# Kernel tuning notes

Hardware: AMD Instinct MI355X
Metric: run time of the kernel (lower is better)

## Reference

```python
import jax, jax.numpy as jnp
import numpy as np

MIN = 1e-30
BLOCK = 64


def setup_inputs() -> dict:
    key = jax.random.key(0)
    ks = jax.random.split(key, 16)
    B, L, D, H, M, E, P, R = 4, 512, 768, 12, 48, 32, 512, 97
    inp = {
        "context": jax.random.normal(ks[0], (B, L, D), jnp.float32),
        "attention": jax.random.uniform(ks[1], (B, H, L, L), jnp.float32),
        "mention_map": jax.random.uniform(ks[2], (B, M, L), jnp.float32),
        "entity_map": jax.random.uniform(ks[3], (B, E, M), jnp.float32),
        "hts": jax.random.randint(ks[4], (B, P, 2), 0, E).astype(jnp.int64),
        "hW": jax.random.normal(ks[5], (D, D), jnp.float32) * 0.02,
        "hb": jnp.zeros((D,), jnp.float32),
        "tW": jax.random.normal(ks[6], (D, D), jnp.float32) * 0.02,
        "tb": jnp.zeros((D,), jnp.float32),
        "hcW": jax.random.normal(ks[7], (D, D), jnp.float32) * 0.02,
        "hcb": jnp.zeros((D,), jnp.float32),
        "tcW": jax.random.normal(ks[8], (D, D), jnp.float32) * 0.02,
        "tcb": jnp.zeros((D,), jnp.float32),
        "clasW": jax.random.normal(ks[9], (R, D * BLOCK), jnp.float32) * 0.02,
        "clasb": jnp.zeros((R,), jnp.float32),
    }
    return inp


def _group_bilinear(h, t, W, b):
    # h, t: [B, P, D]; grouped bilinear a la ATLOP: block-outer-product then linear
    B, P, D = h.shape
    nb = D // BLOCK
    h_ = h.reshape(B, P, nb, BLOCK)
    t_ = t.reshape(B, P, nb, BLOCK)
    feat = jnp.einsum("bpni,bpnj->bpnij", h_, t_).reshape(B, P, D * BLOCK)
    return feat @ W.T + b


def _forward(context, attention, mention_map, entity_map, hts,
             hW, hb, tW, tb, hcW, hcb, tcW, tcb, clasW, clasb):
    B = context.shape[0]
    bidx = jnp.arange(B)[:, None]
    h_idx = hts[..., 0]  # [B, P]
    t_idx = hts[..., 1]
    ht_mask = (hts.sum(-1) != 0)[..., None].astype(context.dtype)  # [B, P, 1]

    # ---- get_ht ----
    mention = mention_map @ context                       # [B, M, D]
    att_sum = attention.sum(axis=1)                       # [B, L, L]
    mention_att = mention_map @ att_sum @ jnp.swapaxes(mention_map, 1, 2)  # [B, M, M]
    entity_att = entity_map @ mention_att                 # [B, E, M]

    h_mask = entity_map[bidx, h_idx] * ht_mask            # [B, P, M]
    t_mask = entity_map[bidx, t_idx] * ht_mask
    h_att = entity_att[bidx, h_idx] * t_mask
    t_att = entity_att[bidx, t_idx] * h_mask
    h_att = h_att / (h_att.sum(-1, keepdims=True) + MIN)
    t_att = t_att / (t_att.sum(-1, keepdims=True) + MIN)
    h = (t_att @ mention) * ht_mask                       # [B, P, D]
    t = (h_att @ mention) * ht_mask

    # ---- context_pooling (entity_map projected to token space) ----
    em_tok = entity_map @ mention_map                     # [B, E, L]
    em_tok = em_tok / (em_tok.sum(-1, keepdims=True) + MIN)
    ent_att = jnp.einsum("bel,bhlm->bhem", em_tok, attention)  # [B, H, E, L]
    hA = ent_att[bidx, :, h_idx]                          # [B, P, H, L]
    tA = ent_att[bidx, :, t_idx]
    ctx_att = (hA * tA).sum(axis=2)                       # [B, P, L]
    ctx_att = ctx_att / (ctx_att.sum(-1, keepdims=True) + MIN)
    context_info = (ctx_att @ context) * ht_mask          # [B, P, D]

    h_info = context_info @ hcW.T + hcb
    t_info = context_info @ tcW.T + tcb
    h = jnp.tanh(h @ hW.T + hb + h_info)
    t = jnp.tanh(t @ tW.T + tb + t_info)
    return _group_bilinear(h, t, clasW, clasb)            # [B, P, R]


def reference(context, attention, mention_map, entity_map, hts,
              hW, hb, tW, tb, hcW, hcb, tcW, tcb, clasW, clasb):
    return _forward(context, attention, mention_map, entity_map, hts,
                    hW, hb, tW, tb, hcW, hcb, tcW, tcb, clasW, clasb)
```

## Files before the change

kernel.cpp:

```cpp
#include <hip/hip_runtime.h>
#include <math.h>

#define Bc 4
#define Lc 512
#define Dc 768
#define Hc 12
#define Mc 48
#define Ec 32
#define Pc 512
#define Rc 97
#define MINV 1e-30f

typedef _Float16 f16;
typedef __attribute__((ext_vector_type(8))) _Float16 f16x8;
typedef __attribute__((ext_vector_type(4))) _Float16 f16x4;
typedef __attribute__((ext_vector_type(16))) float f32x16;

__global__ __launch_bounds__(256) void k_prep(const float* __restrict__ hW, const float* __restrict__ tW,
                                              const float* __restrict__ hcW, const float* __restrict__ tcW,
                                              f16* __restrict__ hWb, f16* __restrict__ tWb,
                                              f16* __restrict__ hcWb, f16* __restrict__ tcWb,
                                              const float* __restrict__ clasW, f16* __restrict__ Wp,
                                              const float* __restrict__ ctx, f16* __restrict__ ctxT,
                                              const float* __restrict__ mm, f16* __restrict__ mmH) {
    __shared__ f16 Ts[64][72];
    int bid = blockIdx.x;
    int tid = threadIdx.x;
    if (bid < 2048) {
        const int DD = Dc * Dc;
        int i = bid * 256 + tid;
        int stride = 2048 * 256;
        for (; i < 4 * DD; i += stride) {
            int sel = i / DD, j = i % DD;
            const float* s = (sel == 0) ? hW : (sel == 1) ? tW : (sel == 2) ? hcW : tcW;
            f16* d = (sel == 0) ? hWb : (sel == 1) ? tWb : (sel == 2) ? hcWb : tcWb;
            d[j] = (f16)s[j];
        }
    } else if (bid < 5120) {
        int gid = (bid - 2048) * 256 + tid;
        int lane = gid & 63; int f = gid >> 6;
        int rt = f & 3; int s = (f >> 2) & 3; int c = f >> 4;
        int n_l = lane & 31, kg = lane >> 5;
        int r = rt * 32 + n_l;
        f16x8 v;
        if (r < Rc) {
            const float* src = clasW + (size_t)r * (Dc * 64) + c * 64 + s * 16 + kg * 8;
#pragma unroll
            for (int j = 0; j < 8; ++j) v[j] = (f16)src[j];
        } else {
#pragma unroll
            for (int j = 0; j < 8; ++j) v[j] = (f16)0.f;
        }
        ((f16x8*)Wp)[gid] = v;
    } else if (bid < 5504) {
        int id = bid - 5120;
        int dt = id % 12; int lt = (id / 12) % 8; int b = id / 96;
        int l0 = lt * 64, d0 = dt * 64;
        int r = tid >> 2, cg = tid & 3;
        const float* src = ctx + ((size_t)b * Lc + l0 + r) * Dc + d0 + cg * 16;
#pragma unroll
        for (int u = 0; u < 4; ++u) {
            float4 v = ((const float4*)src)[u];
            Ts[cg * 16 + u * 4 + 0][r] = (f16)v.x;
            Ts[cg * 16 + u * 4 + 1][r] = (f16)v.y;
            Ts[cg * 16 + u * 4 + 2][r] = (f16)v.z;
            Ts[cg * 16 + u * 4 + 3][r] = (f16)v.w;
        }
        __syncthreads();
        int dr = tid >> 2, seg = tid & 3;
        f16* dst = ctxT + ((size_t)b * Dc + d0 + dr) * Lc + l0 + seg * 16;
        f16x8 o0, o1;
#pragma unroll
        for (int j = 0; j < 8; ++j) { o0[j] = Ts[dr][seg * 16 + j]; o1[j] = Ts[dr][seg * 16 + 8 + j]; }
        *(f16x8*)dst = o0;
        *(f16x8*)(dst + 8) = o1;
    } else {
        int gid = (bid - 5504) * 256 + tid;
        const float4* src = (const float4*)(mm + (size_t)gid * 8);
        float4 v0 = src[0], v1 = src[1];
        f16x8 o;
        o[0] = (f16)v0.x; o[1] = (f16)v0.y; o[2] = (f16)v0.z; o[3] = (f16)v0.w;
        o[4] = (f16)v1.x; o[5] = (f16)v1.y; o[6] = (f16)v1.z; o[7] = (f16)v1.w;
        ((f16x8*)mmH)[gid] = o;
    }
}

__global__ __launch_bounds__(256) void k_mention_mfma(const f16* __restrict__ mmH,
                                                      const f16* __restrict__ ctxT,
                                                      float* __restrict__ mention) {
    __shared__ __align__(16) f16 As[2][64 * 64];
    __shared__ __align__(16) f16 Bs[2][64 * 64];
    int id = blockIdx.x;
    int dt = id % 12; int b = id / 12;
    int d0 = dt * 64;
    int tid = threadIdx.x;
    int w = tid >> 6, lane = tid & 63;
    int w_m = w & 1, w_n = w >> 1;
    int m_l = lane & 31, kg = lane >> 5;
    int r0 = tid >> 3, cc0 = tid & 7;
    int r1 = r0 + 32;
    int mr0 = (r0 < Mc) ? r0 : r0 - Mc;
    int mr1 = (r1 < Mc) ? r1 : r1 - Mc;
    f16x8 ar0, ar1, br0, br1;
    auto loadt = [&](int it) {
        int k0 = it * 64;
        ar0 = *(const f16x8*)(mmH + ((size_t)b * Mc + mr0) * Lc + k0 + cc0 * 8);
        ar1 = *(const f16x8*)(mmH + ((size_t)b * Mc + mr1) * Lc + k0 + cc0 * 8);
        br0 = *(const f16x8*)(ctxT + ((size_t)b * Dc + d0 + r0) * Lc + k0 + cc0 * 8);
        br1 = *(const f16x8*)(ctxT + ((size_t)b * Dc + d0 + r1) * Lc + k0 + cc0 * 8);
    };
    auto writet = [&](int p) {
        ((f16x8*)As[p])[r0 * 8 + (cc0 ^ (r0 & 7))] = ar0;
        ((f16x8*)As[p])[r1 * 8 + (cc0 ^ (r1 & 7))] = ar1;
        ((f16x8*)Bs[p])[r0 * 8 + (cc0 ^ (r0 & 7))] = br0;
        ((f16x8*)Bs[p])[r1 * 8 + (cc0 ^ (r1 & 7))] = br1;
    };
    loadt(0); writet(0); loadt(1);
    f32x16 acc;
#pragma unroll
    for (int i = 0; i < 16; ++i) acc[i] = 0.f;
    int ar = w_m * 32 + m_l;
    int br = w_n * 32 + m_l;
    for (int it = 0; it < 8; ++it) {
        int p = it & 1;
        __syncthreads();
        if (it < 7) writet(p ^ 1);
        if (it < 6) loadt(it + 2);
#pragma unroll
        for (int s = 0; s < 4; ++s) {
            int ck = s * 2 + kg;
            f16x8 a = ((const f16x8*)As[p])[ar * 8 + (ck ^ (ar & 7))];
            f16x8 bv = ((const f16x8*)Bs[p])[br * 8 + (ck ^ (br & 7))];
            acc = __builtin_amdgcn_mfma_f32_32x32x16_f16(a, bv, acc, 0, 0, 0);
        }
    }
#pragma unroll
    for (int reg = 0; reg < 16; ++reg) {
        int row = (reg & 3) + 8 * (reg >> 2) + 4 * kg;
        int m = w_m * 32 + row;
        if (m < Mc) mention[((size_t)b * Mc + m) * Dc + d0 + w_n * 32 + m_l] = acc[reg];
    }
}

__global__ __launch_bounds__(256) void k_attpass(const f16* __restrict__ mmH,
                                                 const f16* __restrict__ emtH,
                                                 const float* __restrict__ att,
                                                 float* __restrict__ tmpML,
                                                 float* __restrict__ eat) {
    __shared__ __align__(16) f16 Ss[96 * 64];
    __shared__ __align__(16) f16 attS[64 * 64];
    int id = blockIdx.x;
    int mt = id & 7; int bh = id >> 3;
    int b = bh / Hc, h = bh % Hc;
    int m0 = mt * 64;
    int tid = threadIdx.x;
    int w = tid >> 6, lane = tid & 63;
    int n_l = lane & 31, kg = lane >> 5;

    const float* ab = att + (size_t)bh * Lc * Lc + m0;
    int mRow = tid & 63, lg = tid >> 6;
    float pre[16];
#pragma unroll
    for (int q = 0; q < 16; ++q) pre[q] = ab[(size_t)(lg * 16 + q) * Lc + mRow];

    f32x16 acc[2];
#pragma unroll
    for (int nt = 0; nt < 2; ++nt)
#pragma unroll
        for (int i = 0; i < 16; ++i) acc[nt][i] = 0.f;

    for (int kc = 0; kc < 8; ++kc) {
        __syncthreads();
#pragma unroll
        for (int half = 0; half < 2; ++half) {
            int cc = lg * 2 + half;
            f16x8 v;
#pragma unroll
            for (int jj = 0; jj < 8; ++jj) v[jj] = (f16)pre[half * 8 + jj];
            ((f16x8*)attS)[mRow * 8 + (cc ^ (mRow & 7))] = v;
        }
#pragma unroll
        for (int k = 0; k < 3; ++k) {
            int idx = tid + k * 256;
            int row = idx >> 3, cc = idx & 7;
            f16x8 v;
            if (row < Mc) {
                v = *(const f16x8*)(mmH + ((size_t)b * Mc + row) * Lc + kc * 64 + cc * 8);
            } else if (row < 80) {
                v = *(const f16x8*)(emtH + ((size_t)b * Ec + row - Mc) * Lc + kc * 64 + cc * 8);
            } else {
#pragma unroll
                for (int j = 0; j < 8; ++j) v[j] = (f16)0.f;
            }
            ((f16x8*)Ss)[row * 8 + (cc ^ (row & 7))] = v;
        }
        if (kc < 7) {
#pragma unroll
            for (int q = 0; q < 16; ++q)
                pre[q] = ab[(size_t)((kc + 1) * 64 + lg * 16 + q) * Lc + mRow];
        }
        __syncthreads();
        if (w < 3) {
            int arow = w * 32 + n_l;
#pragma unroll
            for (int kk = 0; kk < 4; ++kk) {
                int cc = kk * 2 + kg;
                f16x8 a = ((const f16x8*)Ss)[arow * 8 + (cc ^ (arow & 7))];
#pragma unroll
                for (int nt = 0; nt < 2; ++nt) {
                    int bcol = nt * 32 + n_l;
                    f16x8 bb = ((const f16x8*)attS)[bcol * 8 + (cc ^ (bcol & 7))];
                    acc[nt] = __builtin_amdgcn_mfma_f32_32x32x16_f16(a, bb, acc[nt], 0, 0, 0);
                }
            }
        }
    }
    if (w < 3) {
#pragma unroll
        for (int nt = 0; nt < 2; ++nt)
#pragma unroll
            for (int reg = 0; reg < 16; ++reg) {
                int row = (reg & 3) + 8 * (reg >> 2) + 4 * kg;
                int rr = w * 32 + row;
                int col = m0 + nt * 32 + n_l;
                if (rr < Mc) {
                    atomicAdd(&tmpML[((size_t)b * Mc + rr) * Lc + col], acc[nt][reg]);
                } else if (rr < 80) {
                    eat[(((size_t)b * Hc + h) * Ec + (rr - Mc)) * Lc + col] = acc[nt][reg];
                }
            }
    }
}

__global__ __launch_bounds__(256) void k_ma(const float* __restrict__ tmp,
                                            const float* __restrict__ mm,
                                            float* __restrict__ maS) {
    int wv = threadIdx.x >> 6, lane = threadIdx.x & 63;
    int gid = blockIdx.x * 4 + wv;
    int m2 = gid % 48;
    int m  = (gid / 48) % 48;
    int b  = gid / (48 * 48);
    const float4* t = (const float4*)(tmp + ((size_t)b * Mc + m)  * Lc);
    const float4* r = (const float4*)(mm  + ((size_t)b * Mc + m2) * Lc);
    float4 a0 = t[lane],      b0 = r[lane];
    float4 a1 = t[lane + 64], b1 = r[lane + 64];
    float acc = a0.x * b0.x + a0.y * b0.y + a0.z * b0.z + a0.w * b0.w
              + a1.x * b1.x + a1.y * b1.y + a1.z * b1.z + a1.w * b1.w;
#pragma unroll
    for (int off = 1; off < 64; off <<= 1) acc += __shfl_xor(acc, off);
    if (lane == 0) maS[gid] = acc;
}

__global__ __launch_bounds__(256) void k_ea(const float* __restrict__ maS,
                                            const float* __restrict__ em,
                                            float* __restrict__ ea) {
    __shared__ float S[48 * 48];
    int b  = blockIdx.x >> 3;
    int eg = blockIdx.x & 7;
    int tid = threadIdx.x;
    for (int i = tid; i < 48 * 48; i += 256) S[i] = maS[(size_t)b * 48 * 48 + i];
    __syncthreads();
    int wv = tid >> 6, lane = tid & 63;
    int e = eg * 4 + wv;
    if (lane < 48) {
        const float* emr = em + ((size_t)b * Ec + e) * Mc;
        float acc = 0.f;
#pragma unroll
        for (int m = 0; m < 48; ++m) acc += emr[m] * S[m * 48 + lane];
        ea[((size_t)b * Ec + e) * Mc + lane] = acc;
    }
}

__global__ __launch_bounds__(256) void k_pair(const int* __restrict__ hts,
                                              const float* __restrict__ em,
                                              const float* __restrict__ ea,
                                              const float* __restrict__ eat,
                                              f16* __restrict__ hatN, f16* __restrict__ tatN,
                                              f16* __restrict__ caH) {
    int wv = threadIdx.x >> 6, lane = threadIdx.x & 63;
    int bp = blockIdx.x * 4 + wv;
    int b = bp >> 9;
    int hi = hts[bp * 2], ti = hts[bp * 2 + 1];
    float mask = (hi + ti != 0) ? 1.f : 0.f;
    float hat = 0.f, tat = 0.f;
    if (lane < Mc) {
        float hm = em[((size_t)(b * Ec + hi)) * Mc + lane];
        float tm = em[((size_t)(b * Ec + ti)) * Mc + lane];
        float eh = ea[((size_t)(b * Ec + hi)) * Mc + lane];
        float et = ea[((size_t)(b * Ec + ti)) * Mc + lane];
        hat = eh * tm * mask;
        tat = et * hm * mask;
    }
    float sh = hat, st = tat;
#pragma unroll
    for (int off = 1; off < 64; off <<= 1) { sh += __shfl_xor(sh, off); st += __shfl_xor(st, off); }
    float hnorm = 1.f / (sh + MINV);
    float tnorm = 1.f / (st + MINV);
    hatN[(size_t)bp * 64 + lane] = (f16)(hat * hnorm);
    tatN[(size_t)bp * 64 + lane] = (f16)(tat * tnorm);

    const float* base = eat + (size_t)b * Hc * Ec * Lc;
    float prod[8];
    float tot = 0.f;
#pragma unroll
    for (int j8 = 0; j8 < 8; ++j8) {
        int j = j8 * 64 + lane;
        float a = 0.f;
#pragma unroll
        for (int h = 0; h < Hc; ++h)
            a += base[((size_t)h * Ec + hi) * Lc + j] * base[((size_t)h * Ec + ti) * Lc + j];
        prod[j8] = a;
        tot += a;
    }
#pragma unroll
    for (int off = 1; off < 64; off <<= 1) tot += __shfl_xor(tot, off);
    float inv = 1.f / (tot + MINV);
#pragma unroll
    for (int j8 = 0; j8 < 8; ++j8)
        caH[(size_t)bp * Lc + j8 * 64 + lane] = (f16)(prod[j8] * inv);
}

__global__ __launch_bounds__(256) void k_ht_mfma(const f16* __restrict__ tatN, const f16* __restrict__ hatN,
                                                 const float* __restrict__ mention,
                                                 f16* __restrict__ hB, f16* __restrict__ tB) {
    __shared__ __align__(16) f16 At[64 * 64];
    __shared__ __align__(16) f16 Ah[64 * 64];
    __shared__ __align__(16) f16 Bs[64 * 64];
    int m0 = blockIdx.x * 64;
    int b = m0 >> 9;
    int d0 = blockIdx.y * 64;
    int tid = threadIdx.x;
    int w = tid >> 6, lane = tid & 63;
    int w_m = w & 1, w_n = w >> 1;
    int m_l = lane & 31, kg = lane >> 5;

    for (int i = tid; i < 512; i += 256) {
        int p = i >> 3, c = i & 7;
        ((f16x8*)At)[p * 8 + (c ^ (p & 7))] = *(const f16x8*)(tatN + (size_t)(m0 + p) * 64 + c * 8);
        ((f16x8*)Ah)[p * 8 + (c ^ (p & 7))] = *(const f16x8*)(hatN + (size_t)(m0 + p) * 64 + c * 8);
    }
    for (int i = tid; i < 512; i += 256) {
        f16x8 z;
#pragma unroll
        for (int j = 0; j < 8; ++j) z[j] = (f16)0.f;
        ((f16x8*)Bs)[i] = z;
    }
    __syncthreads();
    if (tid < 192) {
        int m = tid >> 2, q = tid & 3;
        const float4* src = (const float4*)(mention + ((size_t)b * Mc + m) * Dc + d0 + q * 16);
#pragma unroll
        for (int u = 0; u < 4; ++u) {
            float4 v = src[u];
            int dl = q * 16 + u * 4;
#pragma unroll
            for (int x = 0; x < 4; ++x) {
                float vv = (x == 0) ? v.x : (x == 1) ? v.y : (x == 2) ? v.z : v.w;
                int d = dl + x;
                Bs[(d * 8 + ((m >> 3) ^ (d & 7))) * 8 + (m & 7)] = (f16)vv;
            }
        }
    }
    __syncthreads();

    f32x16 acch, acct;
#pragma unroll
    for (int i = 0; i < 16; ++i) { acch[i] = 0.f; acct[i] = 0.f; }
    int ar = w_m * 32 + m_l;
    int br = w_n * 32 + m_l;
#pragma unroll
    for (int s = 0; s < 4; ++s) {
        int ck = s * 2 + kg;
        f16x8 at_ = ((const f16x8*)At)[ar * 8 + (ck ^ (ar & 7))];
        f16x8 ah_ = ((const f16x8*)Ah)[ar * 8 + (ck ^ (ar & 7))];
        f16x8 bv = ((const f16x8*)Bs)[br * 8 + (ck ^ (br & 7))];
        acch = __builtin_amdgcn_mfma_f32_32x32x16_f16(at_, bv, acch, 0, 0, 0);
        acct = __builtin_amdgcn_mfma_f32_32x32x16_f16(ah_, bv, acct, 0, 0, 0);
    }
#pragma unroll
    for (int reg = 0; reg < 16; ++reg) {
        int row = (reg & 3) + 8 * (reg >> 2) + 4 * kg;
        int p = m0 + w_m * 32 + row;
        int d = d0 + w_n * 32 + m_l;
        hB[(size_t)p * Dc + d] = (f16)acch[reg];
        tB[(size_t)p * Dc + d] = (f16)acct[reg];
    }
}

__global__ __launch_bounds__(256) void k_emtok(const float* __restrict__ em,
                                               const float* __restrict__ mm,
                                               f16* __restrict__ emtH) {
    int be = blockIdx.x; int b = be / Ec;
    __shared__ float row[Mc];
    __shared__ float red[256];
    __shared__ float inv;
    int tid = threadIdx.x;
    if (tid < Mc) row[tid] = em[(size_t)be * Mc + tid];
    __syncthreads();
    float v0 = 0.f, v1 = 0.f;
    {
        const float* mb0 = mm + (size_t)b * Mc * Lc + tid;
        const float* mb1 = mm + (size_t)b * Mc * Lc + tid + 256;
        for (int m = 0; m < Mc; ++m) {
            v0 += row[m] * mb0[(size_t)m * Lc];
            v1 += row[m] * mb1[(size_t)m * Lc];
        }
    }
    red[tid] = v0 + v1;
    __syncthreads();
    for (int s = 128; s > 0; s >>= 1) { if (tid < s) red[tid] += red[tid + s]; __syncthreads(); }
    if (tid == 0) inv = 1.f / (red[0] + MINV);
    __syncthreads();
    emtH[(size_t)be * Lc + tid] = (f16)(v0 * inv);
    emtH[(size_t)be * Lc + tid + 256] = (f16)(v1 * inv);
}

__global__ __launch_bounds__(256) void k_ctxinfo_mfma(const int* __restrict__ hts,
                                                      const f16* __restrict__ caH,
                                                      const f16* __restrict__ ctxT,
                                                      f16* __restrict__ ci) {
    __shared__ __align__(16) f16 As[2][64 * 64];
    __shared__ __align__(16) f16 Bs[2][64 * 64];
    __shared__ float maskS[64];
    int id = blockIdx.x;
    int dt = id % 12; int pt = (id / 12) % 8; int b = id / 96;
    int p0 = pt * 64, d0 = dt * 64;
    int tid = threadIdx.x;
    int w = tid >> 6, lane = tid & 63;
    int w_m = w & 1, w_n = w >> 1;
    int m_l = lane & 31, kg = lane >> 5;
    int r0 = tid >> 3, cc0 = tid & 7;
    int r1 = r0 + 32;
    if (tid < 64) {
        int bp = b * Pc + p0 + tid;
        maskS[tid] = (hts[bp * 2] + hts[bp * 2 + 1] != 0) ? 1.f : 0.f;
    }
    f16x8 ar0, ar1, br0, br1;
    auto loadt = [&](int it) {
        int k0 = it * 64;
        ar0 = *(const f16x8*)(caH + (size_t)(b * Pc + p0 + r0) * Lc + k0 + cc0 * 8);
        ar1 = *(const f16x8*)(caH + (size_t)(b * Pc + p0 + r1) * Lc + k0 + cc0 * 8);
        br0 = *(const f16x8*)(ctxT + (size_t)(b * Dc + d0 + r0) * Lc + k0 + cc0 * 8);
        br1 = *(const f16x8*)(ctxT + (size_t)(b * Dc + d0 + r1) * Lc + k0 + cc0 * 8);
    };
    auto writet = [&](int p) {
        ((f16x8*)As[p])[r0 * 8 + (cc0 ^ (r0 & 7))] = ar0;
        ((f16x8*)As[p])[r1 * 8 + (cc0 ^ (r1 & 7))] = ar1;
        ((f16x8*)Bs[p])[r0 * 8 + (cc0 ^ (r0 & 7))] = br0;
        ((f16x8*)Bs[p])[r1 * 8 + (cc0 ^ (r1 & 7))] = br1;
    };
    loadt(0); writet(0); loadt(1);
    f32x16 acc;
#pragma unroll
    for (int i = 0; i < 16; ++i) acc[i] = 0.f;
    int ar = w_m * 32 + m_l;
    int br = w_n * 32 + m_l;
    for (int it = 0; it < 8; ++it) {
        int p = it & 1;
        __syncthreads();
        if (it < 7) writet(p ^ 1);
        if (it < 6) loadt(it + 2);
#pragma unroll
        for (int s = 0; s < 4; ++s) {
            int ck = s * 2 + kg;
            f16x8 a = ((const f16x8*)As[p])[ar * 8 + (ck ^ (ar & 7))];
            f16x8 bv = ((const f16x8*)Bs[p])[br * 8 + (ck ^ (br & 7))];
            acc = __builtin_amdgcn_mfma_f32_32x32x16_f16(a, bv, acc, 0, 0, 0);
        }
    }
#pragma unroll
    for (int reg = 0; reg < 16; ++reg) {
        int row = (reg & 3) + 8 * (reg >> 2) + 4 * kg;
        int p = p0 + w_m * 32 + row;
        int d = d0 + w_n * 32 + m_l;
        ci[(size_t)(b * Pc + p) * Dc + d] = (f16)(acc[reg] * maskS[w_m * 32 + row]);
    }
}

__global__ __launch_bounds__(256) void k_proj_mfma(const f16* __restrict__ Xh, const f16* __restrict__ Wh,
                                                   const float* __restrict__ bh,
                                                   const f16* __restrict__ Xt, const f16* __restrict__ Wt,
                                                   const float* __restrict__ bt,
                                                   const f16* __restrict__ Xc, const f16* __restrict__ Whc,
                                                   const float* __restrict__ bhc,
                                                   const f16* __restrict__ Wtc, const float* __restrict__ btc,
                                                   f16* __restrict__ outh, f16* __restrict__ outt) {
    __shared__ __align__(16) f16 Xs[2][64 * 64];
    __shared__ __align__(16) f16 Ws[2][64 * 64];
    int z = blockIdx.z;
    const f16* X1 = z ? Xt : Xh;
    const f16* W1 = z ? Wt : Wh;
    const float* b1 = z ? bt : bh;
    const f16* W2 = z ? Wtc : Whc;
    const float* b2 = z ? btc : bhc;
    f16* outp = z ? outt : outh;
    int m0 = blockIdx.x * 64, n0 = blockIdx.y * 64;
    int tid = threadIdx.x;
    int w = tid >> 6, lane = tid & 63;
    int w_m = w & 1, w_n = w >> 1;
    int m_l = lane & 31, kg = lane >> 5;
    const f16* Xarr[2] = {X1, Xc};
    const f16* Warr[2] = {W1, W2};
    int r0 = tid >> 3, cc0 = tid & 7;
    int r1 = r0 + 32;
    f16x8 xr0, xr1, wr0, wr1;
    auto loadt = [&](int it) {
        int src = it / 12; int k0 = (it % 12) * 64;
        const f16* X = Xarr[src]; const f16* W = Warr[src];
        xr0 = *(const f16x8*)(X + (size_t)(m0 + r0) * Dc + k0 + cc0 * 8);
        xr1 = *(const f16x8*)(X + (size_t)(m0 + r1) * Dc + k0 + cc0 * 8);
        wr0 = *(const f16x8*)(W + (size_t)(n0 + r0) * Dc + k0 + cc0 * 8);
        wr1 = *(const f16x8*)(W + (size_t)(n0 + r1) * Dc + k0 + cc0 * 8);
    };
    auto writet = [&](int p) {
        ((f16x8*)Xs[p])[r0 * 8 + (cc0 ^ (r0 & 7))] = xr0;
        ((f16x8*)Xs[p])[r1 * 8 + (cc0 ^ (r1 & 7))] = xr1;
        ((f16x8*)Ws[p])[r0 * 8 + (cc0 ^ (r0 & 7))] = wr0;
        ((f16x8*)Ws[p])[r1 * 8 + (cc0 ^ (r1 & 7))] = wr1;
    };
    loadt(0); writet(0); loadt(1);
    f32x16 acc;
#pragma unroll
    for (int i = 0; i < 16; ++i) acc[i] = 0.f;
    int ar = w_m * 32 + m_l;
    int br = w_n * 32 + m_l;
    for (int it = 0; it < 24; ++it) {
        int p = it & 1;
        __syncthreads();
        if (it < 23) writet(p ^ 1);
        if (it < 22) loadt(it + 2);
#pragma unroll
        for (int s = 0; s < 4; ++s) {
            int ck = s * 2 + kg;
            f16x8 a = ((const f16x8*)Xs[p])[ar * 8 + (ck ^ (ar & 7))];
            f16x8 b = ((const f16x8*)Ws[p])[br * 8 + (ck ^ (br & 7))];
            acc = __builtin_amdgcn_mfma_f32_32x32x16_f16(a, b, acc, 0, 0, 0);
        }
    }
#pragma unroll
    for (int reg = 0; reg < 16; ++reg) {
        int row = (reg & 3) + 8 * (reg >> 2) + 4 * kg;
        int m = m0 + w_m * 32 + row;
        int n = n0 + w_n * 32 + m_l;
        float v = tanhf(acc[reg] + b1[n] + b2[n]);
        outp[(size_t)m * Dc + n] = (f16)v;
    }
}

__global__ __launch_bounds__(256, 3) void k_bilin6(const f16* __restrict__ hF, const f16* __restrict__ tF,
                                                   const f16* __restrict__ Wp, f16* __restrict__ partial) {
    __shared__ __align__(16) f16 tS[128 * 64];
    __shared__ f16 hS[128 * 17];
    int id = blockIdx.x;
    int tile = id / 48;
    int slice = id % 48;
    int bp0 = tile * 128;
    int tid = threadIdx.x;
    int w = tid >> 6, lane = tid & 63;
    int w_m = w & 1, w_r = w >> 1;
    int m_l = lane & 31, kg = lane >> 5;
    int c0 = slice * 16;
    int n = c0 >> 6;

    for (int idx = tid; idx < 128 * 16; idx += 256) {
        int bp = idx >> 4, i = idx & 15;
        hS[bp * 17 + i] = hF[(size_t)(bp0 + bp) * Dc + c0 + i];
    }
    for (int idx = tid; idx < 128 * 8; idx += 256) {
        int bp = idx >> 3, cc = idx & 7;
        f16x8 tv = *(const f16x8*)(tF + (size_t)(bp0 + bp) * Dc + n * 64 + cc * 8);
        ((f16x8*)tS)[bp * 8 + (cc ^ (bp & 7))] = tv;
    }
    __syncthreads();

    f32x16 acc[2][2];
#pragma unroll
    for (int mt = 0; mt < 2; ++mt)
#pragma unroll
        for (int rt = 0; rt < 2; ++rt)
#pragma unroll
            for (int i = 0; i < 16; ++i) acc[mt][rt][i] = 0.f;

    int rowA = w_m * 64 + m_l;
    int rowB = rowA + 32;
    const f16x8* WpB = (const f16x8*)Wp;

    for (int ii = 0; ii < 16; ++ii) {
        int cc = c0 + ii;
        const f16x8* wpb = WpB + (size_t)cc * 16 * 64 + lane;
        f16x8 Bf[8];
#pragma unroll
        for (int s = 0; s < 4; ++s) {
            Bf[s * 2 + 0] = wpb[(s * 4 + 2 * w_r + 0) * 64];
            Bf[s * 2 + 1] = wpb[(s * 4 + 2 * w_r + 1) * 64];
        }
        f16 hv0 = hS[rowA * 17 + ii];
        f16 hv1 = hS[rowB * 17 + ii];
#pragma unroll
        for (int s = 0; s < 4; ++s) {
            int ck = s * 2 + kg;
            f16x8 tv0 = ((const f16x8*)tS)[rowA * 8 + (ck ^ (rowA & 7))];
            f16x8 tv1 = ((const f16x8*)tS)[rowB * 8 + (ck ^ (rowB & 7))];
            f16x8 a0 = tv0 * hv0;
            f16x8 a1 = tv1 * hv1;
            acc[0][0] = __builtin_amdgcn_mfma_f32_32x32x16_f16(a0, Bf[s * 2 + 0], acc[0][0], 0, 0, 0);
            acc[1][0] = __builtin_amdgcn_mfma_f32_32x32x16_f16(a1, Bf[s * 2 + 0], acc[1][0], 0, 0, 0);
            acc[0][1] = __builtin_amdgcn_mfma_f32_32x32x16_f16(a0, Bf[s * 2 + 1], acc[0][1], 0, 0, 0);
            acc[1][1] = __builtin_amdgcn_mfma_f32_32x32x16_f16(a1, Bf[s * 2 + 1], acc[1][1], 0, 0, 0);
        }
    }

    f16* pbase = partial + (size_t)slice * (2048 * 128);
#pragma unroll
    for (int rt = 0; rt < 2; ++rt) {
        int r = (w_r * 2 + rt) * 32 + m_l;
#pragma unroll
        for (int mt = 0; mt < 2; ++mt)
#pragma unroll
            for (int reg = 0; reg < 16; ++reg) {
                int row = (reg & 3) + 8 * (reg >> 2) + 4 * kg;
                int bp = bp0 + w_m * 64 + mt * 32 + row;
                pbase[(size_t)bp * 128 + r] = (f16)acc[mt][rt][reg];
            }
    }
}

__global__ __launch_bounds__(256) void k_reduce(const f16* __restrict__ partial,
                                                const float* __restrict__ cb,
                                                float* __restrict__ out) {
    int idx = blockIdx.x * 256 + threadIdx.x;
    int bp = idx >> 5, c = idx & 31;
    const f16x4* p = (const f16x4*)partial + idx;
    float a0 = 0.f, a1 = 0.f, a2 = 0.f, a3 = 0.f;
#pragma unroll
    for (int s = 0; s < 48; ++s) {
        f16x4 v = p[(size_t)s * (2048 * 32)];
        a0 += (float)v[0]; a1 += (float)v[1]; a2 += (float)v[2]; a3 += (float)v[3];
    }
    int rb = c * 4;
    float* ob = out + (size_t)bp * Rc;
    if (rb + 0 < Rc) ob[rb + 0] = a0 + cb[rb + 0];
    if (rb + 1 < Rc) ob[rb + 1] = a1 + cb[rb + 1];
    if (rb + 2 < Rc) ob[rb + 2] = a2 + cb[rb + 2];
    if (rb + 3 < Rc) ob[rb + 3] = a3 + cb[rb + 3];
}

extern "C" void kernel_launch(void* const* d_in, const int* in_sizes, int n_in,
                              void* d_out, int out_size, void* d_ws, size_t ws_size,
                              hipStream_t stream) {
    const float* context   = (const float*)d_in[0];
    const float* attention = (const float*)d_in[1];
    const float* mm        = (const float*)d_in[2];
    const float* em        = (const float*)d_in[3];
    const int*   hts       = (const int*)d_in[4];
    const float* hW        = (const float*)d_in[5];
    const float* hb        = (const float*)d_in[6];
    const float* tW        = (const float*)d_in[7];
    const float* tb        = (const float*)d_in[8];
    const float* hcW       = (const float*)d_in[9];
    const float* hcb       = (const float*)d_in[10];
    const float* tcW       = (const float*)d_in[11];
    const float* tcb       = (const float*)d_in[12];
    const float* clasW     = (const float*)d_in[13];
    const float* clasb     = (const float*)d_in[14];
    float* out = (float*)d_out;

    char* wsb = (char*)d_ws;
    auto alloc = [&](size_t bytes) { char* p = wsb; wsb += (bytes + 255) & ~(size_t)255; return p; };
    float* mention     = (float*)alloc((size_t)Bc * Mc * Dc * 4);
    float* tmpML       = (float*)alloc((size_t)Bc * Mc * Lc * 4);
    float* entity_att  = (float*)alloc((size_t)Bc * Ec * Mc * 4);
    float* ent_att     = (float*)alloc((size_t)Bc * Hc * Ec * Lc * 4);
    float* maS         = (float*)alloc((size_t)Bc * Mc * Mc * 4);
    f16* em_tok  = (f16*)alloc((size_t)Bc * Ec * Lc * 2);
    f16* ctx_att = (f16*)alloc((size_t)Bc * Pc * Lc * 2);
    f16* mmH     = (f16*)alloc((size_t)Bc * Mc * Lc * 2);
    f16* hatN    = (f16*)alloc((size_t)Bc * Pc * 64 * 2);
    f16* tatN    = (f16*)alloc((size_t)Bc * Pc * 64 * 2);
    f16* h_buf   = (f16*)alloc((size_t)Bc * Pc * Dc * 2);
    f16* t_buf   = (f16*)alloc((size_t)Bc * Pc * Dc * 2);
    f16* ctxinfo = (f16*)alloc((size_t)Bc * Pc * Dc * 2);
    f16* h_fin   = (f16*)alloc((size_t)Bc * Pc * Dc * 2);
    f16* t_fin   = (f16*)alloc((size_t)Bc * Pc * Dc * 2);
    f16* hWb     = (f16*)alloc((size_t)Dc * Dc * 2);
    f16* tWb     = (f16*)alloc((size_t)Dc * Dc * 2);
    f16* hcWb    = (f16*)alloc((size_t)Dc * Dc * 2);
    f16* tcWb    = (f16*)alloc((size_t)Dc * Dc * 2);
    f16* ctxT    = (f16*)alloc((size_t)Bc * Dc * Lc * 2);
    f16* Wp      = (f16*)alloc((size_t)768 * 16 * 64 * 8 * 2);
    f16* partial = (f16*)alloc((size_t)48 * 2048 * 128 * 2);

    hipMemsetAsync(tmpML, 0, (size_t)Bc * Mc * Lc * 4, stream);
    k_prep<<<dim3(5552), dim3(256), 0, stream>>>(hW, tW, hcW, tcW, hWb, tWb, hcWb, tcWb,
                                                 clasW, Wp, context, ctxT, mm, mmH);
    k_emtok<<<dim3(Bc * Ec), dim3(256), 0, stream>>>(em, mm, em_tok);
    k_attpass<<<dim3(Bc * Hc * 8), dim3(256), 0, stream>>>(mmH, em_tok, attention, tmpML, ent_att);
    k_mention_mfma<<<dim3(Bc * 12), dim3(256), 0, stream>>>(mmH, ctxT, mention);
    k_ma<<<dim3(Bc * Mc * Mc / 4), dim3(256), 0, stream>>>(tmpML, mm, maS);
    k_ea<<<dim3(Bc * 8), dim3(256), 0, stream>>>(maS, em, entity_att);
    k_pair<<<dim3(Bc * Pc / 4), dim3(256), 0, stream>>>(hts, em, entity_att, ent_att, hatN, tatN, ctx_att);
    k_ht_mfma<<<dim3(32, 12), dim3(256), 0, stream>>>(tatN, hatN, mention, h_buf, t_buf);
    k_ctxinfo_mfma<<<dim3(384), dim3(256), 0, stream>>>(hts, ctx_att, ctxT, ctxinfo);
    k_proj_mfma<<<dim3(32, 12, 2), dim3(256), 0, stream>>>(h_buf, hWb, hb, t_buf, tWb, tb,
                                                           ctxinfo, hcWb, hcb, tcWb, tcb, h_fin, t_fin);
    k_bilin6<<<dim3(768), dim3(256), 0, stream>>>(h_fin, t_fin, Wp, partial);
    k_reduce<<<dim3(256), dim3(256), 0, stream>>>(partial, clasb, out);
}
```

Measured before the change: 265.8 us.

## Merge independent kernels into shared launches and retile bilinear kernel

```diff
diff --git a/kernel.cpp b/kernel.cpp
--- a/kernel.cpp
+++ b/kernel.cpp
@@ -10,6 +10,7 @@
 #define Pc 512
 #define Rc 97
 #define MINV 1e-30f
+#define NSLICE 24
 
 typedef _Float16 f16;
 typedef __attribute__((ext_vector_type(8))) _Float16 f16x8;
@@ -22,8 +23,12 @@
                                               f16* __restrict__ hcWb, f16* __restrict__ tcWb,
                                               const float* __restrict__ clasW, f16* __restrict__ Wp,
                                               const float* __restrict__ ctx, f16* __restrict__ ctxT,
-                                              const float* __restrict__ mm, f16* __restrict__ mmH) {
+                                              const float* __restrict__ mm, f16* __restrict__ mmH,
+                                              const float* __restrict__ em, f16* __restrict__ emtH) {
     __shared__ f16 Ts[64][72];
+    __shared__ float rowS[Mc];
+    __shared__ float red[256];
+    __shared__ float inv;
     int bid = blockIdx.x;
     int tid = threadIdx.x;
     if (bid < 2048) {
@@ -74,7 +79,7 @@
         for (int j = 0; j < 8; ++j) { o0[j] = Ts[dr][seg * 16 + j]; o1[j] = Ts[dr][seg * 16 + 8 + j]; }
         *(f16x8*)dst = o0;
         *(f16x8*)(dst + 8) = o1;
-    } else {
+    } else if (bid < 5552) {
         int gid = (bid - 5504) * 256 + tid;
         const float4* src = (const float4*)(mm + (size_t)gid * 8);
         float4 v0 = src[0], v1 = src[1];
@@ -82,153 +87,172 @@
         o[0] = (f16)v0.x; o[1] = (f16)v0.y; o[2] = (f16)v0.z; o[3] = (f16)v0.w;
         o[4] = (f16)v1.x; o[5] = (f16)v1.y; o[6] = (f16)v1.z; o[7] = (f16)v1.w;
         ((f16x8*)mmH)[gid] = o;
-    }
-}
-
-__global__ __launch_bounds__(256) void k_mention_mfma(const f16* __restrict__ mmH,
-                                                      const f16* __restrict__ ctxT,
-                                                      float* __restrict__ mention) {
-    __shared__ __align__(16) f16 As[2][64 * 64];
-    __shared__ __align__(16) f16 Bs[2][64 * 64];
-    int id = blockIdx.x;
-    int dt = id % 12; int b = id / 12;
-    int d0 = dt * 64;
+    } else {
+        int be = bid - 5552; int b = be / Ec;
+        if (tid < Mc) rowS[tid] = em[(size_t)be * Mc + tid];
+        __syncthreads();
+        float v0 = 0.f, v1 = 0.f;
+        {
+            const float* mb0 = mm + (size_t)b * Mc * Lc + tid;
+            const float* mb1 = mm + (size_t)b * Mc * Lc + tid + 256;
+            for (int m = 0; m < Mc; ++m) {
+                v0 += rowS[m] * mb0[(size_t)m * Lc];
+                v1 += rowS[m] * mb1[(size_t)m * Lc];
+            }
+        }
+        red[tid] = v0 + v1;
+        __syncthreads();
+        for (int s = 128; s > 0; s >>= 1) { if (tid < s) red[tid] += red[tid + s]; __syncthreads(); }
+        if (tid == 0) inv = 1.f / (red[0] + MINV);
+        __syncthreads();
+        emtH[(size_t)be * Lc + tid] = (f16)(v0 * inv);
+        emtH[(size_t)be * Lc + tid + 256] = (f16)(v1 * inv);
+    }
+}
+
+__global__ __launch_bounds__(256) void k_att_mention(const f16* __restrict__ mmH,
+                                                     const f16* __restrict__ emtH,
+                                                     const float* __restrict__ att,
+                                                     float* __restrict__ tmpML,
+                                                     float* __restrict__ eat,
+                                                     const f16* __restrict__ ctxT,
+                                                     float* __restrict__ mention) {
+    __shared__ __align__(16) char smem[32768];
+    int bid = blockIdx.x;
     int tid = threadIdx.x;
     int w = tid >> 6, lane = tid & 63;
-    int w_m = w & 1, w_n = w >> 1;
-    int m_l = lane & 31, kg = lane >> 5;
-    int r0 = tid >> 3, cc0 = tid & 7;
-    int r1 = r0 + 32;
-    int mr0 = (r0 < Mc) ? r0 : r0 - Mc;
-    int mr1 = (r1 < Mc) ? r1 : r1 - Mc;
-    f16x8 ar0, ar1, br0, br1;
-    auto loadt = [&](int it) {
-        int k0 = it * 64;
-        ar0 = *(const f16x8*)(mmH + ((size_t)b * Mc + mr0) * Lc + k0 + cc0 * 8);
-        ar1 = *(const f16x8*)(mmH + ((size_t)b * Mc + mr1) * Lc + k0 + cc0 * 8);
-        br0 = *(const f16x8*)(ctxT + ((size_t)b * Dc + d0 + r0) * Lc + k0 + cc0 * 8);
-        br1 = *(const f16x8*)(ctxT + ((size_t)b * Dc + d0 + r1) * Lc + k0 + cc0 * 8);
-    };
-    auto writet = [&](int p) {
-        ((f16x8*)As[p])[r0 * 8 + (cc0 ^ (r0 & 7))] = ar0;
-        ((f16x8*)As[p])[r1 * 8 + (cc0 ^ (r1 & 7))] = ar1;
-        ((f16x8*)Bs[p])[r0 * 8 + (cc0 ^ (r0 & 7))] = br0;
-        ((f16x8*)Bs[p])[r1 * 8 + (cc0 ^ (r1 & 7))] = br1;
-    };
-    loadt(0); writet(0); loadt(1);
-    f32x16 acc;
-#pragma unroll
-    for (int i = 0; i < 16; ++i) acc[i] = 0.f;
-    int ar = w_m * 32 + m_l;
-    int br = w_n * 32 + m_l;
-    for (int it = 0; it < 8; ++it) {
-        int p = it & 1;
-        __syncthreads();
-        if (it < 7) writet(p ^ 1);
-        if (it < 6) loadt(it + 2);
-#pragma unroll
-        for (int s = 0; s < 4; ++s) {
-            int ck = s * 2 + kg;
-            f16x8 a = ((const f16x8*)As[p])[ar * 8 + (ck ^ (ar & 7))];
-            f16x8 bv = ((const f16x8*)Bs[p])[br * 8 + (ck ^ (br & 7))];
-            acc = __builtin_amdgcn_mfma_f32_32x32x16_f16(a, bv, acc, 0, 0, 0);
-        }
-    }
-#pragma unroll
-    for (int reg = 0; reg < 16; ++reg) {
-        int row = (reg & 3) + 8 * (reg >> 2) + 4 * kg;
-        int m = w_m * 32 + row;
-        if (m < Mc) mention[((size_t)b * Mc + m) * Dc + d0 + w_n * 32 + m_l] = acc[reg];
-    }
-}
-
-__global__ __launch_bounds__(256) void k_attpass(const f16* __restrict__ mmH,
-                                                 const f16* __restrict__ emtH,
-                                                 const float* __restrict__ att,
-                                                 float* __restrict__ tmpML,
-                                                 float* __restrict__ eat) {
-    __shared__ __align__(16) f16 Ss[96 * 64];
-    __shared__ __align__(16) f16 attS[64 * 64];
-    int id = blockIdx.x;
-    int mt = id & 7; int bh = id >> 3;
-    int b = bh / Hc, h = bh % Hc;
-    int m0 = mt * 64;
-    int tid = threadIdx.x;
-    int w = tid >> 6, lane = tid & 63;
-    int n_l = lane & 31, kg = lane >> 5;
-
-    const float* ab = att + (size_t)bh * Lc * Lc + m0;
-    int mRow = tid & 63, lg = tid >> 6;
-    float pre[16];
-#pragma unroll
-    for (int q = 0; q < 16; ++q) pre[q] = ab[(size_t)(lg * 16 + q) * Lc + mRow];
-
-    f32x16 acc[2];
-#pragma unroll
-    for (int nt = 0; nt < 2; ++nt)
-#pragma unroll
-        for (int i = 0; i < 16; ++i) acc[nt][i] = 0.f;
-
-    for (int kc = 0; kc < 8; ++kc) {
-        __syncthreads();
-#pragma unroll
-        for (int half = 0; half < 2; ++half) {
-            int cc = lg * 2 + half;
-            f16x8 v;
-#pragma unroll
-            for (int jj = 0; jj < 8; ++jj) v[jj] = (f16)pre[half * 8 + jj];
-            ((f16x8*)attS)[mRow * 8 + (cc ^ (mRow & 7))] = v;
-        }
-#pragma unroll
-        for (int k = 0; k < 3; ++k) {
-            int idx = tid + k * 256;
-            int row = idx >> 3, cc = idx & 7;
-            f16x8 v;
-            if (row < Mc) {
-                v = *(const f16x8*)(mmH + ((size_t)b * Mc + row) * Lc + kc * 64 + cc * 8);
-            } else if (row < 80) {
-                v = *(const f16x8*)(emtH + ((size_t)b * Ec + row - Mc) * Lc + kc * 64 + cc * 8);
-            } else {
-#pragma unroll
-                for (int j = 0; j < 8; ++j) v[j] = (f16)0.f;
-            }
-            ((f16x8*)Ss)[row * 8 + (cc ^ (row & 7))] = v;
-        }
-        if (kc < 7) {
-#pragma unroll
-            for (int q = 0; q < 16; ++q)
-                pre[q] = ab[(size_t)((kc + 1) * 64 + lg * 16 + q) * Lc + mRow];
-        }
-        __syncthreads();
+    if (bid < 384) {
+        f16* Ss   = (f16*)smem;
+        f16* attS = (f16*)(smem + 12288);
+        int mt = bid & 7; int bh = bid >> 3;
+        int b = bh / Hc, h = bh % Hc;
+        int m0 = mt * 64;
+        int n_l = lane & 31, kg = lane >> 5;
+
+        const float* ab = att + (size_t)bh * Lc * Lc + m0;
+        int mRow = tid & 63, lg = tid >> 6;
+        float pre[16];
+#pragma unroll
+        for (int q = 0; q < 16; ++q) pre[q] = ab[(size_t)(lg * 16 + q) * Lc + mRow];
+
+        f32x16 acc[2];
+#pragma unroll
+        for (int nt = 0; nt < 2; ++nt)
+#pragma unroll
+            for (int i = 0; i < 16; ++i) acc[nt][i] = 0.f;
+
+        for (int kc = 0; kc < 8; ++kc) {
+            __syncthreads();
+#pragma unroll
+            for (int half = 0; half < 2; ++half) {
+                int cc = lg * 2 + half;
+                f16x8 v;
+#pragma unroll
+                for (int jj = 0; jj < 8; ++jj) v[jj] = (f16)pre[half * 8 + jj];
+                ((f16x8*)attS)[mRow * 8 + (cc ^ (mRow & 7))] = v;
+            }
+#pragma unroll
+            for (int k = 0; k < 3; ++k) {
+                int idx = tid + k * 256;
+                int row = idx >> 3, cc = idx & 7;
+                f16x8 v;
+                if (row < Mc) {
+                    v = *(const f16x8*)(mmH + ((size_t)b * Mc + row) * Lc + kc * 64 + cc * 8);
+                } else if (row < 80) {
+                    v = *(const f16x8*)(emtH + ((size_t)b * Ec + row - Mc) * Lc + kc * 64 + cc * 8);
+                } else {
+#pragma unroll
+                    for (int j = 0; j < 8; ++j) v[j] = (f16)0.f;
+                }
+                ((f16x8*)Ss)[row * 8 + (cc ^ (row & 7))] = v;
+            }
+            if (kc < 7) {
+#pragma unroll
+                for (int q = 0; q < 16; ++q)
+                    pre[q] = ab[(size_t)((kc + 1) * 64 + lg * 16 + q) * Lc + mRow];
+            }
+            __syncthreads();
+            if (w < 3) {
+                int arow = w * 32 + n_l;
+#pragma unroll
+                for (int kk = 0; kk < 4; ++kk) {
+                    int cc = kk * 2 + kg;
+                    f16x8 a = ((const f16x8*)Ss)[arow * 8 + (cc ^ (arow & 7))];
+#pragma unroll
+                    for (int nt = 0; nt < 2; ++nt) {
+                        int bcol = nt * 32 + n_l;
+                        f16x8 bb = ((const f16x8*)attS)[bcol * 8 + (cc ^ (bcol & 7))];
+                        acc[nt] = __builtin_amdgcn_mfma_f32_32x32x16_f16(a, bb, acc[nt], 0, 0, 0);
+                    }
+                }
+            }
+        }
         if (w < 3) {
-            int arow = w * 32 + n_l;
-#pragma unroll
-            for (int kk = 0; kk < 4; ++kk) {
-                int cc = kk * 2 + kg;
-                f16x8 a = ((const f16x8*)Ss)[arow * 8 + (cc ^ (arow & 7))];
-#pragma unroll
-                for (int nt = 0; nt < 2; ++nt) {
-                    int bcol = nt * 32 + n_l;
-                    f16x8 bb = ((const f16x8*)attS)[bcol * 8 + (cc ^ (bcol & 7))];
-                    acc[nt] = __builtin_amdgcn_mfma_f32_32x32x16_f16(a, bb, acc[nt], 0, 0, 0);
+#pragma unroll
+            for (int nt = 0; nt < 2; ++nt)
+#pragma unroll
+                for (int reg = 0; reg < 16; ++reg) {
+                    int row = (reg & 3) + 8 * (reg >> 2) + 4 * kg;
+                    int rr = w * 32 + row;
+                    int col = m0 + nt * 32 + n_l;
+                    if (rr < Mc) {
+                        atomicAdd(&tmpML[((size_t)b * Mc + rr) * Lc + col], acc[nt][reg]);
+                    } else if (rr < 80) {
+                        eat[(((size_t)b * Hc + h) * Ec + (rr - Mc)) * Lc + col] = acc[nt][reg];
+                    }
                 }
-            }
-        }
-    }
-    if (w < 3) {
-#pragma unroll
-        for (int nt = 0; nt < 2; ++nt)
-#pragma unroll
-            for (int reg = 0; reg < 16; ++reg) {
-                int row = (reg & 3) + 8 * (reg >> 2) + 4 * kg;
-                int rr = w * 32 + row;
-                int col = m0 + nt * 32 + n_l;
-                if (rr < Mc) {
-                    atomicAdd(&tmpML[((size_t)b * Mc + rr) * Lc + col], acc[nt][reg]);
-                } else if (rr < 80) {
-                    eat[(((size_t)b * Hc + h) * Ec + (rr - Mc)) * Lc + col] = acc[nt][reg];
-                }
-            }
+        }
+    } else {
+        f16* As = (f16*)smem;
+        f16* Bs = (f16*)(smem + 16384);
+        int id = bid - 384;
+        int dt = id % 12; int b = id / 12;
+        int d0 = dt * 64;
+        int w_m = w & 1, w_n = w >> 1;
+        int m_l = lane & 31, kg = lane >> 5;
+        int r0 = tid >> 3, cc0 = tid & 7;
+        int r1 = r0 + 32;
+        int mr0 = (r0 < Mc) ? r0 : r0 - Mc;
+        int mr1 = (r1 < Mc) ? r1 : r1 - Mc;
+        f16x8 ar0, ar1, br0, br1;
+        auto loadt = [&](int it) {
+            int k0 = it * 64;
+            ar0 = *(const f16x8*)(mmH + ((size_t)b * Mc + mr0) * Lc + k0 + cc0 * 8);
+            ar1 = *(const f16x8*)(mmH + ((size_t)b * Mc + mr1) * Lc + k0 + cc0 * 8);
+            br0 = *(const f16x8*)(ctxT + ((size_t)b * Dc + d0 + r0) * Lc + k0 + cc0 * 8);
+            br1 = *(const f16x8*)(ctxT + ((size_t)b * Dc + d0 + r1) * Lc + k0 + cc0 * 8);
+        };
+        auto writet = [&](int p) {
+            ((f16x8*)(As + p * 4096))[r0 * 8 + (cc0 ^ (r0 & 7))] = ar0;
+            ((f16x8*)(As + p * 4096))[r1 * 8 + (cc0 ^ (r1 & 7))] = ar1;
+            ((f16x8*)(Bs + p * 4096))[r0 * 8 + (cc0 ^ (r0 & 7))] = br0;
+            ((f16x8*)(Bs + p * 4096))[r1 * 8 + (cc0 ^ (r1 & 7))] = br1;
+        };
+        loadt(0); writet(0); loadt(1);
+        f32x16 acc;
+#pragma unroll
+        for (int i = 0; i < 16; ++i) acc[i] = 0.f;
+        int ar = w_m * 32 + m_l;
+        int br = w_n * 32 + m_l;
+        for (int it = 0; it < 8; ++it) {
+            int p = it & 1;
+            __syncthreads();
+            if (it < 7) writet(p ^ 1);
+            if (it < 6) loadt(it + 2);
+#pragma unroll
+            for (int s = 0; s < 4; ++s) {
+                int ck = s * 2 + kg;
+                f16x8 a = ((const f16x8*)(As + p * 4096))[ar * 8 + (ck ^ (ar & 7))];
+                f16x8 bv = ((const f16x8*)(Bs + p * 4096))[br * 8 + (ck ^ (br & 7))];
+                acc = __builtin_amdgcn_mfma_f32_32x32x16_f16(a, bv, acc, 0, 0, 0);
+            }
+        }
+#pragma unroll
+        for (int reg = 0; reg < 16; ++reg) {
+            int row = (reg & 3) + 8 * (reg >> 2) + 4 * kg;
+            int m = w_m * 32 + row;
+            if (m < Mc) mention[((size_t)b * Mc + m) * Dc + d0 + w_n * 32 + m_l] = acc[reg];
+        }
     }
 }
 
@@ -320,160 +344,131 @@
         caH[(size_t)bp * Lc + j8 * 64 + lane] = (f16)(prod[j8] * inv);
 }
 
-__global__ __launch_bounds__(256) void k_ht_mfma(const f16* __restrict__ tatN, const f16* __restrict__ hatN,
-                                                 const float* __restrict__ mention,
-                                                 f16* __restrict__ hB, f16* __restrict__ tB) {
-    __shared__ __align__(16) f16 At[64 * 64];
-    __shared__ __align__(16) f16 Ah[64 * 64];
-    __shared__ __align__(16) f16 Bs[64 * 64];
-    int m0 = blockIdx.x * 64;
-    int b = m0 >> 9;
-    int d0 = blockIdx.y * 64;
+__global__ __launch_bounds__(256) void k_htci(const f16* __restrict__ tatN, const f16* __restrict__ hatN,
+                                              const float* __restrict__ mention,
+                                              f16* __restrict__ hB, f16* __restrict__ tB,
+                                              const int* __restrict__ hts,
+                                              const f16* __restrict__ caH,
+                                              const f16* __restrict__ ctxT,
+                                              f16* __restrict__ ci) {
+    __shared__ __align__(16) char smem[33024];
+    int bid = blockIdx.x;
     int tid = threadIdx.x;
     int w = tid >> 6, lane = tid & 63;
     int w_m = w & 1, w_n = w >> 1;
     int m_l = lane & 31, kg = lane >> 5;
-
-    for (int i = tid; i < 512; i += 256) {
-        int p = i >> 3, c = i & 7;
-        ((f16x8*)At)[p * 8 + (c ^ (p & 7))] = *(const f16x8*)(tatN + (size_t)(m0 + p) * 64 + c * 8);
-        ((f16x8*)Ah)[p * 8 + (c ^ (p & 7))] = *(const f16x8*)(hatN + (size_t)(m0 + p) * 64 + c * 8);
-    }
-    for (int i = tid; i < 512; i += 256) {
-        f16x8 z;
-#pragma unroll
-        for (int j = 0; j < 8; ++j) z[j] = (f16)0.f;
-        ((f16x8*)Bs)[i] = z;
-    }
-    __syncthreads();
-    if (tid < 192) {
-        int m = tid >> 2, q = tid & 3;
-        const float4* src = (const float4*)(mention + ((size_t)b * Mc + m) * Dc + d0 + q * 16);
-#pragma unroll
-        for (int u = 0; u < 4; ++u) {
-            float4 v = src[u];
-            int dl = q * 16 + u * 4;
-#pragma unroll
-            for (int x = 0; x < 4; ++x) {
-                float vv = (x == 0) ? v.x : (x == 1) ? v.y : (x == 2) ? v.z : v.w;
-                int d = dl + x;
-                Bs[(d * 8 + ((m >> 3) ^ (d & 7))) * 8 + (m & 7)] = (f16)vv;
-            }
-        }
-    }
-    __syncthreads();
-
-    f32x16 acch, acct;
-#pragma unroll
-    for (int i = 0; i < 16; ++i) { acch[i] = 0.f; acct[i] = 0.f; }
-    int ar = w_m * 32 + m_l;
-    int br = w_n * 32 + m_l;
-#pragma unroll
-    for (int s = 0; s < 4; ++s) {
-        int ck = s * 2 + kg;
-        f16x8 at_ = ((const f16x8*)At)[ar * 8 + (ck ^ (ar & 7))];
-        f16x8 ah_ = ((const f16x8*)Ah)[ar * 8 + (ck ^ (ar & 7))];
-        f16x8 bv = ((const f16x8*)Bs)[br * 8 + (ck ^ (br & 7))];
-        acch = __builtin_amdgcn_mfma_f32_32x32x16_f16(at_, bv, acch, 0, 0, 0);
-        acct = __builtin_amdgcn_mfma_f32_32x32x16_f16(ah_, bv, acct, 0, 0, 0);
-    }
-#pragma unroll
-    for (int reg = 0; reg < 16; ++reg) {
-        int row = (reg & 3) + 8 * (reg >> 2) + 4 * kg;
-        int p = m0 + w_m * 32 + row;
-        int d = d0 + w_n * 32 + m_l;
-        hB[(size_t)p * Dc + d] = (f16)acch[reg];
-        tB[(size_t)p * Dc + d] = (f16)acct[reg];
-    }
-}
-
-__global__ __launch_bounds__(256) void k_emtok(const float* __restrict__ em,
-                                               const float* __restrict__ mm,
-                                               f16* __restrict__ emtH) {
-    int be = blockIdx.x; int b = be / Ec;
-    __shared__ float row[Mc];
-    __shared__ float red[256];
-    __shared__ float inv;
-    int tid = threadIdx.x;
-    if (tid < Mc) row[tid] = em[(size_t)be * Mc + tid];
-    __syncthreads();
-    float v0 = 0.f, v1 = 0.f;
-    {
-        const float* mb0 = mm + (size_t)b * Mc * Lc + tid;
-        const float* mb1 = mm + (size_t)b * Mc * Lc + tid + 256;
-        for (int m = 0; m < Mc; ++m) {
-            v0 += row[m] * mb0[(size_t)m * Lc];
-            v1 += row[m] * mb1[(size_t)m * Lc];
-        }
-    }
-    red[tid] = v0 + v1;
-    __syncthreads();
-    for (int s = 128; s > 0; s >>= 1) { if (tid < s) red[tid] += red[tid + s]; __syncthreads(); }
-    if (tid == 0) inv = 1.f / (red[0] + MINV);
-    __syncthreads();
-    emtH[(size_t)be * Lc + tid] = (f16)(v0 * inv);
-    emtH[(size_t)be * Lc + tid + 256] = (f16)(v1 * inv);
-}
-
-__global__ __launch_bounds__(256) void k_ctxinfo_mfma(const int* __restrict__ hts,
-                                                      const f16* __restrict__ caH,
-                                                      const f16* __restrict__ ctxT,
-                                                      f16* __restrict__ ci) {
-    __shared__ __align__(16) f16 As[2][64 * 64];
-    __shared__ __align__(16) f16 Bs[2][64 * 64];
-    __shared__ float maskS[64];
-    int id = blockIdx.x;
-    int dt = id % 12; int pt = (id / 12) % 8; int b = id / 96;
-    int p0 = pt * 64, d0 = dt * 64;
-    int tid = threadIdx.x;
-    int w = tid >> 6, lane = tid & 63;
-    int w_m = w & 1, w_n = w >> 1;
-    int m_l = lane & 31, kg = lane >> 5;
-    int r0 = tid >> 3, cc0 = tid & 7;
-    int r1 = r0 + 32;
-    if (tid < 64) {
-        int bp = b * Pc + p0 + tid;
-        maskS[tid] = (hts[bp * 2] + hts[bp * 2 + 1] != 0) ? 1.f : 0.f;
-    }
-    f16x8 ar0, ar1, br0, br1;
-    auto loadt = [&](int it) {
-        int k0 = it * 64;
-        ar0 = *(const f16x8*)(caH + (size_t)(b * Pc + p0 + r0) * Lc + k0 + cc0 * 8);
-        ar1 = *(const f16x8*)(caH + (size_t)(b * Pc + p0 + r1) * Lc + k0 + cc0 * 8);
-        br0 = *(const f16x8*)(ctxT + (size_t)(b * Dc + d0 + r0) * Lc + k0 + cc0 * 8);
-        br1 = *(const f16x8*)(ctxT + (size_t)(b * Dc + d0 + r1) * Lc + k0 + cc0 * 8);
-    };
-    auto writet = [&](int p) {
-        ((f16x8*)As[p])[r0 * 8 + (cc0 ^ (r0 & 7))] = ar0;
-        ((f16x8*)As[p])[r1 * 8 + (cc0 ^ (r1 & 7))] = ar1;
-        ((f16x8*)Bs[p])[r0 * 8 + (cc0 ^ (r0 & 7))] = br0;
-        ((f16x8*)Bs[p])[r1 * 8 + (cc0 ^ (r1 & 7))] = br1;
-    };
-    loadt(0); writet(0); loadt(1);
-    f32x16 acc;
-#pragma unroll
-    for (int i = 0; i < 16; ++i) acc[i] = 0.f;
-    int ar = w_m * 32 + m_l;
-    int br = w_n * 32 + m_l;
-    for (int it = 0; it < 8; ++it) {
-        int p = it & 1;
+    if (bid < 384) {
+        f16* At = (f16*)smem;
+        f16* Ah = (f16*)(smem + 8192);
+        f16* Bs = (f16*)(smem + 16384);
+        int m0 = (bid & 31) * 64;
+        int b = m0 >> 9;
+        int d0 = (bid >> 5) * 64;
+
+        for (int i = tid; i < 512; i += 256) {
+            int p = i >> 3, c = i & 7;
+            ((f16x8*)At)[p * 8 + (c ^ (p & 7))] = *(const f16x8*)(tatN + (size_t)(m0 + p) * 64 + c * 8);
+            ((f16x8*)Ah)[p * 8 + (c ^ (p & 7))] = *(const f16x8*)(hatN + (size_t)(m0 + p) * 64 + c * 8);
+        }
+        for (int i = tid; i < 512; i += 256) {
+            f16x8 z;
+#pragma unroll
+            for (int j = 0; j < 8; ++j) z[j] = (f16)0.f;
+            ((f16x8*)Bs)[i] = z;
+        }
         __syncthreads();
-        if (it < 7) writet(p ^ 1);
-        if (it < 6) loadt(it + 2);
+        if (tid < 192) {
+            int m = tid >> 2, q = tid & 3;
+            const float4* src = (const float4*)(mention + ((size_t)b * Mc + m) * Dc + d0 + q * 16);
+#pragma unroll
+            for (int u = 0; u < 4; ++u) {
+                float4 v = src[u];
+                int dl = q * 16 + u * 4;
+#pragma unroll
+                for (int x = 0; x < 4; ++x) {
+                    float vv = (x == 0) ? v.x : (x == 1) ? v.y : (x == 2) ? v.z : v.w;
+                    int d = dl + x;
+                    Bs[(d * 8 + ((m >> 3) ^ (d & 7))) * 8 + (m & 7)] = (f16)vv;
+                }
+            }
+        }
+        __syncthreads();
+
+        f32x16 acch, acct;
+#pragma unroll
+        for (int i = 0; i < 16; ++i) { acch[i] = 0.f; acct[i] = 0.f; }
+        int ar = w_m * 32 + m_l;
+        int br = w_n * 32 + m_l;
 #pragma unroll
         for (int s = 0; s < 4; ++s) {
             int ck = s * 2 + kg;
-            f16x8 a = ((const f16x8*)As[p])[ar * 8 + (ck ^ (ar & 7))];
-            f16x8 bv = ((const f16x8*)Bs[p])[br * 8 + (ck ^ (br & 7))];
-            acc = __builtin_amdgcn_mfma_f32_32x32x16_f16(a, bv, acc, 0, 0, 0);
-        }
-    }
-#pragma unroll
-    for (int reg = 0; reg < 16; ++reg) {
-        int row = (reg & 3) + 8 * (reg >> 2) + 4 * kg;
-        int p = p0 + w_m * 32 + row;
-        int d = d0 + w_n * 32 + m_l;
-        ci[(size_t)(b * Pc + p) * Dc + d] = (f16)(acc[reg] * maskS[w_m * 32 + row]);
+            f16x8 at_ = ((const f16x8*)At)[ar * 8 + (ck ^ (ar & 7))];
+            f16x8 ah_ = ((const f16x8*)Ah)[ar * 8 + (ck ^ (ar & 7))];
+            f16x8 bv = ((const f16x8*)Bs)[br * 8 + (ck ^ (br & 7))];
+            acch = __builtin_amdgcn_mfma_f32_32x32x16_f16(at_, bv, acch, 0, 0, 0);
+            acct = __builtin_amdgcn_mfma_f32_32x32x16_f16(ah_, bv, acct, 0, 0, 0);
+        }
+#pragma unroll
+        for (int reg = 0; reg < 16; ++reg) {
+            int row = (reg & 3) + 8 * (reg >> 2) + 4 * kg;
+            int p = m0 + w_m * 32 + row;
+            int d = d0 + w_n * 32 + m_l;
+            hB[(size_t)p * Dc + d] = (f16)acch[reg];
+            tB[(size_t)p * Dc + d] = (f16)acct[reg];
+        }
+    } else {
+        f16* As = (f16*)smem;
+        f16* Bs = (f16*)(smem + 16384);
+        float* maskS = (float*)(smem + 32768);
+        int id = bid - 384;
+        int dt = id % 12; int pt = (id / 12) % 8; int b = id / 96;
+        int p0 = pt * 64, d0 = dt * 64;
+        int r0 = tid >> 3, cc0 = tid & 7;
+        int r1 = r0 + 32;
+        if (tid < 64) {
+            int bp = b * Pc + p0 + tid;
+            maskS[tid] = (hts[bp * 2] + hts[bp * 2 + 1] != 0) ? 1.f : 0.f;
+        }
+        f16x8 ar0, ar1, br0, br1;
+        auto loadt = [&](int it) {
+            int k0 = it * 64;
+            ar0 = *(const f16x8*)(caH + (size_t)(b * Pc + p0 + r0) * Lc + k0 + cc0 * 8);
+            ar1 = *(const f16x8*)(caH + (size_t)(b * Pc + p0 + r1) * Lc + k0 + cc0 * 8);
+            br0 = *(const f16x8*)(ctxT + (size_t)(b * Dc + d0 + r0) * Lc + k0 + cc0 * 8);
+            br1 = *(const f16x8*)(ctxT + (size_t)(b * Dc + d0 + r1) * Lc + k0 + cc0 * 8);
+        };
+        auto writet = [&](int p) {
+            ((f16x8*)(As + p * 4096))[r0 * 8 + (cc0 ^ (r0 & 7))] = ar0;
+            ((f16x8*)(As + p * 4096))[r1 * 8 + (cc0 ^ (r1 & 7))] = ar1;
+            ((f16x8*)(Bs + p * 4096))[r0 * 8 + (cc0 ^ (r0 & 7))] = br0;
+            ((f16x8*)(Bs + p * 4096))[r1 * 8 + (cc0 ^ (r1 & 7))] = br1;
+        };
+        loadt(0); writet(0); loadt(1);
+        f32x16 acc;
+#pragma unroll
+        for (int i = 0; i < 16; ++i) acc[i] = 0.f;
+        int ar = w_m * 32 + m_l;
+        int br = w_n * 32 + m_l;
+        for (int it = 0; it < 8; ++it) {
+            int p = it & 1;
+            __syncthreads();
+            if (it < 7) writet(p ^ 1);
+            if (it < 6) loadt(it + 2);
+#pragma unroll
+            for (int s = 0; s < 4; ++s) {
+                int ck = s * 2 + kg;
+                f16x8 a = ((const f16x8*)(As + p * 4096))[ar * 8 + (ck ^ (ar & 7))];
+                f16x8 bv = ((const f16x8*)(Bs + p * 4096))[br * 8 + (ck ^ (br & 7))];
+                acc = __builtin_amdgcn_mfma_f32_32x32x16_f16(a, bv, acc, 0, 0, 0);
+            }
+        }
+#pragma unroll
+        for (int reg = 0; reg < 16; ++reg) {
+            int row = (reg & 3) + 8 * (reg >> 2) + 4 * kg;
+            int p = p0 + w_m * 32 + row;
+            int d = d0 + w_n * 32 + m_l;
+            ci[(size_t)(b * Pc + p) * Dc + d] = (f16)(acc[reg] * maskS[w_m * 32 + row]);
+        }
     }
 }
 
@@ -547,45 +542,42 @@
     }
 }
 
-__global__ __launch_bounds__(256, 3) void k_bilin6(const f16* __restrict__ hF, const f16* __restrict__ tF,
-                                                   const f16* __restrict__ Wp, f16* __restrict__ partial) {
-    __shared__ __align__(16) f16 tS[128 * 64];
-    __shared__ f16 hS[128 * 17];
+__global__ __launch_bounds__(256, 3) void k_bilin(const f16* __restrict__ hF, const f16* __restrict__ tF,
+                                                  const f16* __restrict__ Wp, f16* __restrict__ partial) {
+    __shared__ __align__(16) f16 tS[64 * 64];
+    __shared__ f16 hS[64 * 33];
     int id = blockIdx.x;
-    int tile = id / 48;
-    int slice = id % 48;
-    int bp0 = tile * 128;
+    int tile = id / NSLICE;
+    int slice = id % NSLICE;
+    int bp0 = tile * 64;
     int tid = threadIdx.x;
     int w = tid >> 6, lane = tid & 63;
     int w_m = w & 1, w_r = w >> 1;
     int m_l = lane & 31, kg = lane >> 5;
-    int c0 = slice * 16;
+    int c0 = slice * 32;
     int n = c0 >> 6;
 
-    for (int idx = tid; idx < 128 * 16; idx += 256) {
-        int bp = idx >> 4, i = idx & 15;
-        hS[bp * 17 + i] = hF[(size_t)(bp0 + bp) * Dc + c0 + i];
-    }
-    for (int idx = tid; idx < 128 * 8; idx += 256) {
+    for (int idx = tid; idx < 64 * 32; idx += 256) {
+        int bp = idx >> 5, i = idx & 31;
+        hS[bp * 33 + i] = hF[(size_t)(bp0 + bp) * Dc + c0 + i];
+    }
+    for (int idx = tid; idx < 64 * 8; idx += 256) {
         int bp = idx >> 3, cc = idx & 7;
         f16x8 tv = *(const f16x8*)(tF + (size_t)(bp0 + bp) * Dc + n * 64 + cc * 8);
         ((f16x8*)tS)[bp * 8 + (cc ^ (bp & 7))] = tv;
     }
     __syncthreads();
 
-    f32x16 acc[2][2];
-#pragma unroll
-    for (int mt = 0; mt < 2; ++mt)
-#pragma unroll
-        for (int rt = 0; rt < 2; ++rt)
-#pragma unroll
-            for (int i = 0; i < 16; ++i) acc[mt][rt][i] = 0.f;
-
-    int rowA = w_m * 64 + m_l;
-    int rowB = rowA + 32;
+    f32x16 acc[2];
+#pragma unroll
+    for (int rt = 0; rt < 2; ++rt)
+#pragma unroll
+        for (int i = 0; i < 16; ++i) acc[rt][i] = 0.f;
+
+    int rowA = w_m * 32 + m_l;
     const f16x8* WpB = (const f16x8*)Wp;
 
-    for (int ii = 0; ii < 16; ++ii) {
+    for (int ii = 0; ii < 32; ++ii) {
         int cc = c0 + ii;
         const f16x8* wpb = WpB + (size_t)cc * 16 * 64 + lane;
         f16x8 Bf[8];
@@ -594,19 +586,14 @@
             Bf[s * 2 + 0] = wpb[(s * 4 + 2 * w_r + 0) * 64];
             Bf[s * 2 + 1] = wpb[(s * 4 + 2 * w_r + 1) * 64];
         }
-        f16 hv0 = hS[rowA * 17 + ii];
-        f16 hv1 = hS[rowB * 17 + ii];
+        f16 hv0 = hS[rowA * 33 + ii];
 #pragma unroll
         for (int s = 0; s < 4; ++s) {
             int ck = s * 2 + kg;
             f16x8 tv0 = ((const f16x8*)tS)[rowA * 8 + (ck ^ (rowA & 7))];
-            f16x8 tv1 = ((const f16x8*)tS)[rowB * 8 + (ck ^ (rowB & 7))];
             f16x8 a0 = tv0 * hv0;
-            f16x8 a1 = tv1 * hv1;
-            acc[0][0] = __builtin_amdgcn_mfma_f32_32x32x16_f16(a0, Bf[s * 2 + 0], acc[0][0], 0, 0, 0);
-            acc[1][0] = __builtin_amdgcn_mfma_f32_32x32x16_f16(a1, Bf[s * 2 + 0], acc[1][0], 0, 0, 0);
-            acc[0][1] = __builtin_amdgcn_mfma_f32_32x32x16_f16(a0, Bf[s * 2 + 1], acc[0][1], 0, 0, 0);
-            acc[1][1] = __builtin_amdgcn_mfma_f32_32x32x16_f16(a1, Bf[s * 2 + 1], acc[1][1], 0, 0, 0);
+            acc[0] = __builtin_amdgcn_mfma_f32_32x32x16_f16(a0, Bf[s * 2 + 0], acc[0], 0, 0, 0);
+            acc[1] = __builtin_amdgcn_mfma_f32_32x32x16_f16(a0, Bf[s * 2 + 1], acc[1], 0, 0, 0);
         }
     }
 
@@ -615,13 +602,11 @@
     for (int rt = 0; rt < 2; ++rt) {
         int r = (w_r * 2 + rt) * 32 + m_l;
 #pragma unroll
-        for (int mt = 0; mt < 2; ++mt)
-#pragma unroll
-            for (int reg = 0; reg < 16; ++reg) {
-                int row = (reg & 3) + 8 * (reg >> 2) + 4 * kg;
-                int bp = bp0 + w_m * 64 + mt * 32 + row;
-                pbase[(size_t)bp * 128 + r] = (f16)acc[mt][rt][reg];
-            }
+        for (int reg = 0; reg < 16; ++reg) {
+            int row = (reg & 3) + 8 * (reg >> 2) + 4 * kg;
+            int bp = bp0 + w_m * 32 + row;
+            pbase[(size_t)bp * 128 + r] = (f16)acc[rt][reg];
+        }
     }
 }
 
@@ -633,7 +618,7 @@
     const f16x4* p = (const f16x4*)partial + idx;
     float a0 = 0.f, a1 = 0.f, a2 = 0.f, a3 = 0.f;
 #pragma unroll
-    for (int s = 0; s < 48; ++s) {
+    for (int s = 0; s < NSLICE; ++s) {
         f16x4 v = p[(size_t)s * (2048 * 32)];
         a0 += (float)v[0]; a1 += (float)v[1]; a2 += (float)v[2]; a3 += (float)v[3];
     }
@@ -688,21 +673,20 @@
     f16* tcWb    = (f16*)alloc((size_t)Dc * Dc * 2);
     f16* ctxT    = (f16*)alloc((size_t)Bc * Dc * Lc * 2);
     f16* Wp      = (f16*)alloc((size_t)768 * 16 * 64 * 8 * 2);
-    f16* partial = (f16*)alloc((size_t)48 * 2048 * 128 * 2);
+    f16* partial = (f16*)alloc((size_t)NSLICE * 2048 * 128 * 2);
 
     hipMemsetAsync(tmpML, 0, (size_t)Bc * Mc * Lc * 4, stream);
-    k_prep<<<dim3(5552), dim3(256), 0, stream>>>(hW, tW, hcW, tcW, hWb, tWb, hcWb, tcWb,
-                                                 clasW, Wp, context, ctxT, mm, mmH);
-    k_emtok<<<dim3(Bc * Ec), dim3(256), 0, stream>>>(em, mm, em_tok);
-    k_attpass<<<dim3(Bc * Hc * 8), dim3(256), 0, stream>>>(mmH, em_tok, attention, tmpML, ent_att);
-    k_mention_mfma<<<dim3(Bc * 12), dim3(256), 0, stream>>>(mmH, ctxT, mention);
+    k_prep<<<dim3(5680), dim3(256), 0, stream>>>(hW, tW, hcW, tcW, hWb, tWb, hcWb, tcWb,
+                                                 clasW, Wp, context, ctxT, mm, mmH, em, em_tok);
+    k_att_mention<<<dim3(432), dim3(256), 0, stream>>>(mmH, em_tok, attention, tmpML, ent_att,
+                                                       ctxT, mention);
     k_ma<<<dim3(Bc * Mc * Mc / 4), dim3(256), 0, stream>>>(tmpML, mm, maS);
     k_ea<<<dim3(Bc * 8), dim3(256), 0, stream>>>(maS, em, entity_att);
     k_pair<<<dim3(Bc * Pc / 4), dim3(256), 0, stream>>>(hts, em, entity_att, ent_att, hatN, tatN, ctx_att);
-    k_ht_mfma<<<dim3(32, 12), dim3(256), 0, stream>>>(tatN, hatN, mention, h_buf, t_buf);
-    k_ctxinfo_mfma<<<dim3(384), dim3(256), 0, stream>>>(hts, ctx_att, ctxT, ctxinfo);
+    k_htci<<<dim3(768), dim3(256), 0, stream>>>(tatN, hatN, mention, h_buf, t_buf,
+                                                hts, ctx_att, ctxT, ctxinfo);
     k_proj_mfma<<<dim3(32, 12, 2), dim3(256), 0, stream>>>(h_buf, hWb, hb, t_buf, tWb, tb,
                                                            ctxinfo, hcWb, hcb, tcWb, tcb, h_fin, t_fin);
-    k_bilin6<<<dim3(768), dim3(256), 0, stream>>>(h_fin, t_fin, Wp, partial);
+    k_bilin<<<dim3(32 * NSLICE), dim3(256), 0, stream>>>(h_fin, t_fin, Wp, partial);
     k_reduce<<<dim3(256), dim3(256), 0, stream>>>(partial, clasb, out);
 }
```

Measured after the change: 250.5 us. 1.06x faster.
